# Kernel optimization log

Measured on AMD Instinct MI355X. Metric: run time of the kernel, lower is better.

Reference implementation:

```python
import jax, jax.numpy as jnp
import numpy as np

B, S, D = 4, 4096, 64
NEG = -1e9  # matches masked_fill(-1000000000.0)


def setup_inputs() -> dict:
    key = jax.random.key(0)
    ks = jax.random.split(key, 10)
    inp = {
        "E": jax.random.normal(ks[0], (B, S, D), jnp.float32),
        "P_K_emb": jax.random.normal(ks[1], (B, S, D), jnp.float32),
        "P_V_emb": jax.random.normal(ks[2], (B, S, D), jnp.float32),
        "Wq": jax.random.normal(ks[3], (D, D), jnp.float32) * (1.0 / np.sqrt(D)),
        "bq": jax.random.normal(ks[4], (D,), jnp.float32) * 0.02,
        "Wk": jax.random.normal(ks[5], (D, D), jnp.float32) * (1.0 / np.sqrt(D)),
        "bk": jax.random.normal(ks[6], (D,), jnp.float32) * 0.02,
        "Wv": jax.random.normal(ks[7], (D, D), jnp.float32) * (1.0 / np.sqrt(D)),
        "bv": jax.random.normal(ks[8], (D,), jnp.float32) * 0.02,
        "pad_mask": jax.random.randint(ks[9], (B, S), 0, 2).astype(jnp.bool_),
    }
    return inp


def reference(E, P_K_emb, P_V_emb, Wq, bq, Wk, bk, Wv, bv, pad_mask):
    d = E.shape[-1]
    # torch nn.Linear: y = x @ W.T + b
    Q = E @ Wq.T + bq                       # [B,S,D]
    K = E @ Wk.T + bk
    V = E @ Wv.T + bv
    K_p = K * P_K_emb                       # popularity-modulated keys
    V_p = V * P_V_emb                       # popularity-modulated values
    scores = jnp.einsum('bqd,bkd->bqk', Q, K_p) / jnp.sqrt(jnp.float32(d))  # [B,S,S]
    S_len = E.shape[1]
    causal = jnp.triu(jnp.ones((S_len, S_len), jnp.bool_), k=1)             # [S,S]
    mask = pad_mask[:, None, :] | causal[None, :, :]                        # [B,S,S]
    scores = jnp.where(mask, jnp.float32(NEG), scores)
    attn = jax.nn.softmax(scores, axis=-1)
    O_I = jnp.einsum('bqk,bkd->bqd', attn, V_p)  # [B,S,D]
    return O_I
```

## Files before the change

### kernel.cpp

```cpp
#include <hip/hip_runtime.h>
#include <hip/hip_bf16.h>

#define Bn 4
#define Sn 4096
#define Dn 64

typedef short          s16x8 __attribute__((ext_vector_type(8)));
typedef unsigned short u16x8 __attribute__((ext_vector_type(8)));
typedef float          f32x4 __attribute__((ext_vector_type(4)));

typedef __attribute__((address_space(1))) const void gas_void;
typedef __attribute__((address_space(3))) void       las_void;

__device__ __forceinline__ unsigned short f2bf(float f) {
    unsigned u = __float_as_uint(f);
    u = u + 0x7fffu + ((u >> 16) & 1u);
    return (unsigned short)(u >> 16);
}
__device__ __forceinline__ float bf2f(unsigned short h) {
    return __uint_as_float(((unsigned)h) << 16);
}
__device__ __forceinline__ unsigned long long pack4(float4 x) {
    return (unsigned long long)f2bf(x.x)
         | ((unsigned long long)f2bf(x.y) << 16)
         | ((unsigned long long)f2bf(x.z) << 32)
         | ((unsigned long long)f2bf(x.w) << 48);
}
__device__ __forceinline__ void gld16(const void* g, void* l) {
    __builtin_amdgcn_global_load_lds((gas_void*)g, (las_void*)l, 16, 0, 0);
}

__global__ void LPSAN_mask_kernel(const unsigned char* pm, unsigned long long* padbits) {
    __shared__ unsigned nzs;
    const int t = threadIdx.x;
    if (t == 0) nzs = 0u;
    __syncthreads();
    const uint4* p4 = (const uint4*)pm;
    unsigned acc = 0;
    #pragma unroll
    for (int k = 0; k < 4; ++k) {
        uint4 x = p4[t + k * 256];
        acc |= (x.x & 0xFFFFFF00u) | (x.y & 0xFFFFFF00u) |
               (x.z & 0xFFFFFF00u) | (x.w & 0xFFFFFF00u);
    }
    if (acc) atomicOr(&nzs, 1u);
    __syncthreads();
    unsigned long long bits = 0ull;
    if (nzs) {
        #pragma unroll
        for (int k = 0; k < 4; ++k) {
            uint4 x = p4[t * 4 + k];
            unsigned w[4] = { x.x, x.y, x.z, x.w };
            #pragma unroll
            for (int wi = 0; wi < 4; ++wi)
                #pragma unroll
                for (int bb = 0; bb < 4; ++bb)
                    bits |= (unsigned long long)(((w[wi] >> (8 * bb)) & 0xFFu) != 0u)
                            << (k * 16 + wi * 4 + bb);
        }
    } else {
        #pragma unroll
        for (int k = 0; k < 16; ++k) {
            uint4 x = p4[t * 16 + k];
            bits |= (unsigned long long)(x.x != 0u) << (k * 4);
            bits |= (unsigned long long)(x.y != 0u) << (k * 4 + 1);
            bits |= (unsigned long long)(x.z != 0u) << (k * 4 + 2);
            bits |= (unsigned long long)(x.w != 0u) << (k * 4 + 3);
        }
    }
    padbits[t] = bits;
}

__global__ void LPSAN_proj_kernel(
    const float* __restrict__ E, const float* __restrict__ PK, const float* __restrict__ PV,
    const float* __restrict__ Wq, const float* __restrict__ bq,
    const float* __restrict__ Wk, const float* __restrict__ bk,
    const float* __restrict__ Wv, const float* __restrict__ bv,
    unsigned short* __restrict__ Qb, unsigned short* __restrict__ Kb,
    unsigned short* __restrict__ Vt, float* __restrict__ meanVsum)
{
    __shared__ unsigned short Ebf[4096];
    __shared__ unsigned short Wbf[3][4096];
    __shared__ unsigned short Tbuf[64 * 72];

    const int t = threadIdx.x;
    const int r0 = blockIdx.x * 64;
    const int b  = r0 >> 12;
    const int s0 = r0 & (Sn - 1);
    const int w = t >> 6, lane = t & 63;
    const int fq = lane >> 4, fr = lane & 15;

    {
        const float4* Eg = (const float4*)(E + (size_t)r0 * 64);
        #pragma unroll
        for (int v = 0; v < 4; ++v) {
            int f = t + v * 256;
            float4 x = Eg[f];
            int row = f >> 4, c4 = f & 15;
            *(unsigned long long*)((char*)Ebf + row * 128 + ((c4 * 8) ^ ((row & 7) << 4))) = pack4(x);
        }
        #pragma unroll
        for (int m = 0; m < 3; ++m) {
            const float4* Wg = (const float4*)(m == 0 ? Wq : m == 1 ? Wk : Wv);
            #pragma unroll
            for (int v = 0; v < 4; ++v) {
                int f = t + v * 256;
                float4 x = Wg[f];
                int row = f >> 4, c4 = f & 15;
                *(unsigned long long*)((char*)Wbf[m] + row * 128 + ((c4 * 8) ^ ((row & 7) << 4))) = pack4(x);
            }
        }
    }
    __syncthreads();

    const int  arow = w * 16 + fr;
    const int  swz  = (fr & 7) << 4;
    const char* Ec = (const char*)Ebf;
    const s16x8 ea0 = *(const s16x8*)(Ec + arow * 128 + ((fq * 16) ^ swz));
    const s16x8 ea1 = *(const s16x8*)(Ec + arow * 128 + ((64 + fq * 16) ^ swz));

    const int sl0 = w * 16 + fq * 4;

    for (int m = 0; m < 3; ++m) {
        const char*  Wc   = (const char*)Wbf[m];
        const float* bias = (m == 0) ? bq : (m == 1) ? bk : bv;

        f32x4 acc[4];
        #pragma unroll
        for (int ct = 0; ct < 4; ++ct) {
            const int brow = ct * 16 + fr;
            s16x8 b0 = *(const s16x8*)(Wc + brow * 128 + ((fq * 16) ^ swz));
            s16x8 b1 = *(const s16x8*)(Wc + brow * 128 + ((64 + fq * 16) ^ swz));
            f32x4 z = f32x4{0.f, 0.f, 0.f, 0.f};
            z = __builtin_amdgcn_mfma_f32_16x16x32_bf16(ea0, b0, z, 0, 0, 0);
            z = __builtin_amdgcn_mfma_f32_16x16x32_bf16(ea1, b1, z, 0, 0, 0);
            acc[ct] = z;
        }

        if (m < 2) {
            #pragma unroll
            for (int ct = 0; ct < 4; ++ct) {
                const int j = ct * 16 + fr;
                const float bb = bias[j];
                if (m == 0) {
                    #pragma unroll
                    for (int r = 0; r < 4; ++r)
                        Tbuf[(sl0 + r) * 72 + j] = f2bf((acc[ct][r] + bb) * 0.125f);
                } else {
                    #pragma unroll
                    for (int r = 0; r < 4; ++r) {
                        float mod = PK[(size_t)(r0 + sl0 + r) * 64 + j];
                        Tbuf[(sl0 + r) * 72 + j] = f2bf((acc[ct][r] + bb) * mod);
                    }
                }
            }
            __syncthreads();
            {
                unsigned short* dst = (m == 0 ? Qb : Kb)
                    + (size_t)(b * Sn + s0 + (t >> 2)) * 64 + (t & 3) * 16;
                u16x8 o0 = *(const u16x8*)&Tbuf[(t >> 2) * 72 + (t & 3) * 16];
                u16x8 o1 = *(const u16x8*)&Tbuf[(t >> 2) * 72 + (t & 3) * 16 + 8];
                *(u16x8*)dst = o0;
                *(u16x8*)(dst + 8) = o1;
            }
            __syncthreads();
        } else {
            #pragma unroll
            for (int ct = 0; ct < 4; ++ct) {
                const int j = ct * 16 + fr;
                const float bb = bias[j];
                unsigned long long pk = 0;
                #pragma unroll
                for (int r = 0; r < 4; ++r) {
                    float mod = PV[(size_t)(r0 + sl0 + r) * 64 + j];
                    pk |= (unsigned long long)f2bf((acc[ct][r] + bb) * mod) << (16 * r);
                }
                *(unsigned long long*)&Tbuf[j * 72 + sl0] = pk;
            }
            __syncthreads();
            {
                const int d = t >> 2, seg = t & 3;
                u16x8 o0 = *(const u16x8*)&Tbuf[d * 72 + seg * 16];
                u16x8 o1 = *(const u16x8*)&Tbuf[d * 72 + seg * 16 + 8];
                unsigned short* dst = Vt + (size_t)(b * 64 + d) * Sn + s0 + seg * 16;
                *(u16x8*)dst = o0;
                *(u16x8*)(dst + 8) = o1;
                float s = 0.f;
                #pragma unroll
                for (int i = 0; i < 8; ++i) s += bf2f(o0[i]) + bf2f(o1[i]);
                s += __shfl_xor(s, 1);
                s += __shfl_xor(s, 2);
                if ((t & 3) == 0) atomicAdd(&meanVsum[b * 64 + d], s);
            }
        }
    }
}

__global__ void LPSAN_attn_kernel(
    const unsigned short* __restrict__ Qb, const unsigned short* __restrict__ Kb,
    const unsigned short* __restrict__ Vt, const unsigned long long* __restrict__ padbits,
    unsigned short* __restrict__ Onorm, float* __restrict__ Lp)
{
    __shared__ unsigned short Klds[2][4096];
    __shared__ unsigned short Vlds[2][4096];
    __shared__ unsigned short Plds[4][1024];

    int id = blockIdx.x, g = 0, base = 0;
    while (id >= base + 8 * (g + 1)) { base += 8 * (g + 1); ++g; }
    const int rel = id - base;
    const int qt = 8 * g + rel / (g + 1);
    const int c  = rel % (g + 1);

    const int b = blockIdx.y;
    const int q0 = qt * 64;
    const int t0 = c * 8;
    const int tcnt = min(8, qt + 1 - t0);
    const int tid = threadIdx.x;
    const int w = tid >> 6, lane = tid & 63;
    const int fq = lane >> 4, fr = lane & 15;
    const int qw = q0 + w * 16;

    const unsigned short* Kbase = Kb + b * (Sn * Dn);
    const unsigned short* Vbase = Vt + b * (Dn * Sn);

    const s16x8 qf0 = *(const s16x8*)(Qb + (b * Sn + qw + fr) * 64 + fq * 8);
    const s16x8 qf1 = *(const s16x8*)(Qb + (b * Sn + qw + fr) * 64 + 32 + fq * 8);

    s16x8 onesb;
    #pragma unroll
    for (int i = 0; i < 8; ++i) onesb[i] = (short)0x3F80;

    f32x4 Oa[4];
    f32x4 lacc = f32x4{0.f, 0.f, 0.f, 0.f};
    #pragma unroll
    for (int i = 0; i < 4; ++i) Oa[i] = f32x4{0.f, 0.f, 0.f, 0.f};

    char* Pw = (char*)&Plds[w][0];

    auto STAGE = [&](int kv0, int bufi) {
        #pragma unroll
        for (int cc = 0; cc < 2; ++cc) {
            int pos = w * 2048 + cc * 1024 + lane * 16;
            int row = pos >> 7;
            int cs  = pos & 127;
            int cl  = cs ^ ((row & 7) << 4);
            gld16(Kbase + (kv0 + row) * 64 + (cl >> 1),
                  (char*)&Klds[bufi][0] + w * 2048 + cc * 1024);
            gld16(Vbase + row * Sn + kv0 + (cl >> 1),
                  (char*)&Vlds[bufi][0] + w * 2048 + cc * 1024);
        }
    };

    auto COMPUTE = [&](int t, int bufi, bool causal) {
        const char* Kc = (const char*)&Klds[bufi][0];
        const char* Vc = (const char*)&Vlds[bufi][0];
        const int kv0 = t * 64;

        f32x4 sc[4];
        #pragma unroll
        for (int tl = 0; tl < 4; ++tl) {
            int row = tl * 16 + fr;
            int swz = (row & 7) << 4;
            s16x8 k0 = *(const s16x8*)(Kc + row * 128 + ((fq * 16) ^ swz));
            s16x8 k1 = *(const s16x8*)(Kc + row * 128 + ((64 + fq * 16) ^ swz));
            f32x4 z = f32x4{0.f, 0.f, 0.f, 0.f};
            z = __builtin_amdgcn_mfma_f32_16x16x32_bf16(qf0, k0, z, 0, 0, 0);
            z = __builtin_amdgcn_mfma_f32_16x16x32_bf16(qf1, k1, z, 0, 0, 0);
            sc[tl] = z;
        }

        const unsigned long long bits = padbits[b * 64 + t];
        #pragma unroll
        for (int tl = 0; tl < 4; ++tl) {
            const bool pad = (bits >> (tl * 16 + fr)) & 1ull;
            const int col = kv0 + tl * 16 + fr;
            #pragma unroll
            for (int r = 0; r < 4; ++r) {
                float p = __expf(sc[tl][r] - 16.0f);
                bool msk = pad || (causal && (col > (qw + fq * 4 + r)));
                sc[tl][r] = msk ? 0.f : p;
            }
        }

        #pragma unroll
        for (int tl = 0; tl < 4; ++tl) {
            #pragma unroll
            for (int r = 0; r < 4; ++r) {
                int prow = fq * 4 + r;
                int pcb = (tl * 16 + fr) * 2;
                *(unsigned short*)(Pw + prow * 128 + (pcb ^ ((prow & 7) << 4))) = f2bf(sc[tl][r]);
            }
        }
        asm volatile("s_waitcnt lgkmcnt(0)" ::: "memory");
        __builtin_amdgcn_sched_barrier(0);

        s16x8 pa0 = *(const s16x8*)(Pw + fr * 128 + ((fq * 16) ^ ((fr & 7) << 4)));
        s16x8 pa1 = *(const s16x8*)(Pw + fr * 128 + ((64 + fq * 16) ^ ((fr & 7) << 4)));
        lacc = __builtin_amdgcn_mfma_f32_16x16x32_bf16(pa0, onesb, lacc, 0, 0, 0);
        lacc = __builtin_amdgcn_mfma_f32_16x16x32_bf16(pa1, onesb, lacc, 0, 0, 0);
        #pragma unroll
        for (int dt = 0; dt < 4; ++dt) {
            int row = dt * 16 + fr;
            int swz = (row & 7) << 4;
            s16x8 v0 = *(const s16x8*)(Vc + row * 128 + ((fq * 16) ^ swz));
            s16x8 v1 = *(const s16x8*)(Vc + row * 128 + ((64 + fq * 16) ^ swz));
            Oa[dt] = __builtin_amdgcn_mfma_f32_16x16x32_bf16(pa0, v0, Oa[dt], 0, 0, 0);
            Oa[dt] = __builtin_amdgcn_mfma_f32_16x16x32_bf16(pa1, v1, Oa[dt], 0, 0, 0);
        }
    };

    STAGE(t0 * 64, 0);
    asm volatile("s_waitcnt vmcnt(0)" ::: "memory");
    __builtin_amdgcn_s_barrier();
    int cur = 0;
    for (int i = 0; i < tcnt - 1; ++i) {
        STAGE((t0 + i + 1) * 64, cur ^ 1);
        COMPUTE(t0 + i, cur, false);
        asm volatile("s_waitcnt vmcnt(0)" ::: "memory");
        __builtin_amdgcn_s_barrier();
        cur ^= 1;
    }
    COMPUTE(t0 + tcnt - 1, cur, (t0 + tcnt - 1) == qt);

    const int slot = (b * 64 + qt) * 8 + c;
    #pragma unroll
    for (int r = 0; r < 4; ++r) {
        int row16 = w * 16 + fq * 4 + r;
        float l = lacc[r];
        float inv = (l > 0.f) ? 1.0f / l : 0.f;
        #pragma unroll
        for (int dt = 0; dt < 4; ++dt)
            Onorm[slot * 4096 + row16 * 64 + dt * 16 + fr] = f2bf(Oa[dt][r] * inv);
        if (fr == 0) Lp[slot * 64 + row16] = l;
    }
}

__global__ void LPSAN_combine_kernel(
    const unsigned short* __restrict__ Onorm, const float* __restrict__ Lp,
    const float* __restrict__ meanVsum, float* __restrict__ out)
{
    const int qt = blockIdx.x, b = blockIdx.y;
    const int nch = (qt >> 3) + 1;
    const int t = threadIdx.x;
    const int row = t >> 2, q4 = t & 3;
    const int slotbase = (b * 64 + qt) * 8;

    float wsum = 0.f, wgt[8];
    for (int c = 0; c < nch; ++c) { wgt[c] = Lp[(slotbase + c) * 64 + row]; wsum += wgt[c]; }
    const bool dead = !(wsum > 0.f);

    float acc[16];
    #pragma unroll
    for (int j = 0; j < 16; ++j) acc[j] = 0.f;
    for (int c = 0; c < nch; ++c) {
        const unsigned short* src = Onorm + (slotbase + c) * 4096 + row * 64 + q4 * 16;
        u16x8 a0 = *(const u16x8*)(src);
        u16x8 a1 = *(const u16x8*)(src + 8);
        #pragma unroll
        for (int j = 0; j < 8; ++j) { acc[j] += wgt[c] * bf2f(a0[j]); acc[j + 8] += wgt[c] * bf2f(a1[j]); }
    }

    const float inv = dead ? 0.f : 1.0f / wsum;
    float4 o[4];
    #pragma unroll
    for (int v = 0; v < 4; ++v) {
        #pragma unroll
        for (int j = 0; j < 4; ++j) {
            int d = q4 * 16 + v * 4 + j;
            float val = dead ? meanVsum[b * 64 + d] * (1.0f / (float)Sn) : acc[v * 4 + j] * inv;
            ((float*)&o[v])[j] = val;
        }
    }
    float* dst = out + ((size_t)(b * Sn + qt * 64 + row) * 64 + q4 * 16);
    #pragma unroll
    for (int v = 0; v < 4; ++v) *(float4*)(dst + v * 4) = o[v];
}

extern "C" void kernel_launch(void* const* d_in, const int* in_sizes, int n_in,
                              void* d_out, int out_size, void* d_ws, size_t ws_size,
                              hipStream_t stream) {
    const float* E  = (const float*)d_in[0];
    const float* PK = (const float*)d_in[1];
    const float* PV = (const float*)d_in[2];
    const float* Wq = (const float*)d_in[3];
    const float* bq = (const float*)d_in[4];
    const float* Wk = (const float*)d_in[5];
    const float* bk = (const float*)d_in[6];
    const float* Wv = (const float*)d_in[7];
    const float* bv = (const float*)d_in[8];
    const unsigned char* pm = (const unsigned char*)d_in[9];

    char* ws = (char*)d_ws;
    const size_t SZ = (size_t)Bn * Sn * Dn * sizeof(unsigned short);
    unsigned short* Qb = (unsigned short*)(ws);
    unsigned short* Kb = (unsigned short*)(ws + SZ);
    unsigned short* Vt = (unsigned short*)(ws + 2 * SZ);
    unsigned short* On = (unsigned short*)(ws + 3 * SZ);
    const size_t ONB = (size_t)Bn * 64 * 8 * 4096 * sizeof(unsigned short);
    float* Lp = (float*)(ws + 3 * SZ + ONB);
    unsigned long long* padbits = (unsigned long long*)(ws + 3 * SZ + ONB + 524288);
    float* meanVsum = (float*)(ws + 3 * SZ + ONB + 524288 + 4096);
    float* out = (float*)d_out;

    hipMemsetAsync(meanVsum, 0, Bn * 64 * sizeof(float), stream);
    hipLaunchKernelGGL(LPSAN_mask_kernel, dim3(1), dim3(256), 0, stream, pm, padbits);
    hipLaunchKernelGGL(LPSAN_proj_kernel, dim3(Bn * Sn / 64), dim3(256), 0, stream,
                       E, PK, PV, Wq, bq, Wk, bk, Wv, bv, Qb, Kb, Vt, meanVsum);
    hipLaunchKernelGGL(LPSAN_attn_kernel, dim3(288, Bn), dim3(256), 0, stream,
                       Qb, Kb, Vt, padbits, On, Lp);
    hipLaunchKernelGGL(LPSAN_combine_kernel, dim3(64, Bn), dim3(256), 0, stream,
                       On, Lp, meanVsum, out);
}
```

Before: 122.2 us.

## Fold memset into parallel mask kernel, reverse attention tile order, direct-write single-chunk tiles

Replaces the memset plus single-block mask kernel with one 9-block init kernel that zeroes meanVsum and builds the pad bitmask in parallel. The attention grid is walked in reverse so the longest causal tiles start first, which should even out the tail. Query tiles with a single key chunk (qt<8) now write normalized fp32 output straight to out, including the mean-V fallback for fully masked rows, so the combine kernel skips them. This cuts launch overhead and some intermediate traffic, at the cost of extra branching in the attention epilogue.

```diff
diff --git a/kernel.cpp b/kernel.cpp
--- a/kernel.cpp
+++ b/kernel.cpp
@@ -30,45 +30,49 @@
     __builtin_amdgcn_global_load_lds((gas_void*)g, (las_void*)l, 16, 0, 0);
 }
 
-__global__ void LPSAN_mask_kernel(const unsigned char* pm, unsigned long long* padbits) {
+__global__ void LPSAN_init_kernel(const unsigned char* pm, unsigned long long* padbits,
+                                  float* meanVsum) {
+    const int k = blockIdx.x, t = threadIdx.x;
+    if (k == 8) { meanVsum[t] = 0.f; return; }
+
     __shared__ unsigned nzs;
-    const int t = threadIdx.x;
     if (t == 0) nzs = 0u;
     __syncthreads();
-    const uint4* p4 = (const uint4*)pm;
-    unsigned acc = 0;
-    #pragma unroll
-    for (int k = 0; k < 4; ++k) {
-        uint4 x = p4[t + k * 256];
-        acc |= (x.x & 0xFFFFFF00u) | (x.y & 0xFFFFFF00u) |
-               (x.z & 0xFFFFFF00u) | (x.w & 0xFFFFFF00u);
-    }
-    if (acc) atomicOr(&nzs, 1u);
+    {
+        const uint2* p2 = (const uint2*)(pm + k * 2048);
+        uint2 x = p2[t];
+        unsigned acc = (x.x & 0xFFFFFF00u) | (x.y & 0xFFFFFF00u);
+        if (acc) atomicOr(&nzs, 1u);
+    }
     __syncthreads();
+    if (t >= 32) return;
+    const int wi = k * 32 + t;
     unsigned long long bits = 0ull;
     if (nzs) {
-        #pragma unroll
-        for (int k = 0; k < 4; ++k) {
-            uint4 x = p4[t * 4 + k];
+        const uint4* p4 = (const uint4*)(pm + wi * 64);
+        #pragma unroll
+        for (int q = 0; q < 4; ++q) {
+            uint4 x = p4[q];
             unsigned w[4] = { x.x, x.y, x.z, x.w };
             #pragma unroll
-            for (int wi = 0; wi < 4; ++wi)
+            for (int wj = 0; wj < 4; ++wj)
                 #pragma unroll
                 for (int bb = 0; bb < 4; ++bb)
-                    bits |= (unsigned long long)(((w[wi] >> (8 * bb)) & 0xFFu) != 0u)
-                            << (k * 16 + wi * 4 + bb);
+                    bits |= (unsigned long long)(((w[wj] >> (8 * bb)) & 0xFFu) != 0u)
+                            << (q * 16 + wj * 4 + bb);
         }
     } else {
-        #pragma unroll
-        for (int k = 0; k < 16; ++k) {
-            uint4 x = p4[t * 16 + k];
-            bits |= (unsigned long long)(x.x != 0u) << (k * 4);
-            bits |= (unsigned long long)(x.y != 0u) << (k * 4 + 1);
-            bits |= (unsigned long long)(x.z != 0u) << (k * 4 + 2);
-            bits |= (unsigned long long)(x.w != 0u) << (k * 4 + 3);
-        }
-    }
-    padbits[t] = bits;
+        const uint4* p4 = (const uint4*)pm + wi * 16;
+        #pragma unroll
+        for (int q = 0; q < 16; ++q) {
+            uint4 x = p4[q];
+            bits |= (unsigned long long)(x.x != 0u) << (q * 4);
+            bits |= (unsigned long long)(x.y != 0u) << (q * 4 + 1);
+            bits |= (unsigned long long)(x.z != 0u) << (q * 4 + 2);
+            bits |= (unsigned long long)(x.w != 0u) << (q * 4 + 3);
+        }
+    }
+    padbits[wi] = bits;
 }
 
 __global__ void LPSAN_proj_kernel(
@@ -199,13 +203,14 @@
 __global__ void LPSAN_attn_kernel(
     const unsigned short* __restrict__ Qb, const unsigned short* __restrict__ Kb,
     const unsigned short* __restrict__ Vt, const unsigned long long* __restrict__ padbits,
-    unsigned short* __restrict__ Onorm, float* __restrict__ Lp)
+    const float* __restrict__ meanVsum,
+    unsigned short* __restrict__ Onorm, float* __restrict__ Lp, float* __restrict__ out)
 {
     __shared__ unsigned short Klds[2][4096];
     __shared__ unsigned short Vlds[2][4096];
     __shared__ unsigned short Plds[4][1024];
 
-    int id = blockIdx.x, g = 0, base = 0;
+    int id = 287 - blockIdx.x, g = 0, base = 0;
     while (id >= base + 8 * (g + 1)) { base += 8 * (g + 1); ++g; }
     const int rel = id - base;
     const int qt = 8 * g + rel / (g + 1);
@@ -322,16 +327,33 @@
     }
     COMPUTE(t0 + tcnt - 1, cur, (t0 + tcnt - 1) == qt);
 
-    const int slot = (b * 64 + qt) * 8 + c;
-    #pragma unroll
-    for (int r = 0; r < 4; ++r) {
-        int row16 = w * 16 + fq * 4 + r;
-        float l = lacc[r];
-        float inv = (l > 0.f) ? 1.0f / l : 0.f;
-        #pragma unroll
-        for (int dt = 0; dt < 4; ++dt)
-            Onorm[slot * 4096 + row16 * 64 + dt * 16 + fr] = f2bf(Oa[dt][r] * inv);
-        if (fr == 0) Lp[slot * 64 + row16] = l;
+    if (qt < 8) {
+        #pragma unroll
+        for (int r = 0; r < 4; ++r) {
+            int qrow = qw + fq * 4 + r;
+            float l = lacc[r];
+            bool dead = !(l > 0.f);
+            float inv = dead ? 0.f : 1.0f / l;
+            #pragma unroll
+            for (int dt = 0; dt < 4; ++dt) {
+                int d = dt * 16 + fr;
+                float val = dead ? meanVsum[b * 64 + d] * (1.0f / (float)Sn)
+                                 : Oa[dt][r] * inv;
+                out[((size_t)(b * Sn + qrow)) * 64 + d] = val;
+            }
+        }
+    } else {
+        const int slot = (b * 64 + qt) * 8 + c;
+        #pragma unroll
+        for (int r = 0; r < 4; ++r) {
+            int row16 = w * 16 + fq * 4 + r;
+            float l = lacc[r];
+            float inv = (l > 0.f) ? 1.0f / l : 0.f;
+            #pragma unroll
+            for (int dt = 0; dt < 4; ++dt)
+                Onorm[slot * 4096 + row16 * 64 + dt * 16 + fr] = f2bf(Oa[dt][r] * inv);
+            if (fr == 0) Lp[slot * 64 + row16] = l;
+        }
     }
 }
 
@@ -339,7 +361,7 @@
     const unsigned short* __restrict__ Onorm, const float* __restrict__ Lp,
     const float* __restrict__ meanVsum, float* __restrict__ out)
 {
-    const int qt = blockIdx.x, b = blockIdx.y;
+    const int qt = 8 + blockIdx.x, b = blockIdx.y;
     const int nch = (qt >> 3) + 1;
     const int t = threadIdx.x;
     const int row = t >> 2, q4 = t & 3;
@@ -402,12 +424,11 @@
     float* meanVsum = (float*)(ws + 3 * SZ + ONB + 524288 + 4096);
     float* out = (float*)d_out;
 
-    hipMemsetAsync(meanVsum, 0, Bn * 64 * sizeof(float), stream);
-    hipLaunchKernelGGL(LPSAN_mask_kernel, dim3(1), dim3(256), 0, stream, pm, padbits);
+    hipLaunchKernelGGL(LPSAN_init_kernel, dim3(9), dim3(256), 0, stream, pm, padbits, meanVsum);
     hipLaunchKernelGGL(LPSAN_proj_kernel, dim3(Bn * Sn / 64), dim3(256), 0, stream,
                        E, PK, PV, Wq, bq, Wk, bk, Wv, bv, Qb, Kb, Vt, meanVsum);
     hipLaunchKernelGGL(LPSAN_attn_kernel, dim3(288, Bn), dim3(256), 0, stream,
-                       Qb, Kb, Vt, padbits, On, Lp);
-    hipLaunchKernelGGL(LPSAN_combine_kernel, dim3(64, Bn), dim3(256), 0, stream,
+                       Qb, Kb, Vt, padbits, meanVsum, On, Lp, out);
+    hipLaunchKernelGGL(LPSAN_combine_kernel, dim3(56, Bn), dim3(256), 0, stream,
                        On, Lp, meanVsum, out);
 }
```

Result: faster. 118.8 us (-2.7%).
